# Optimization experiments

Measured on AMD Instinct MI355X. Metric: run time of the kernel, lower is better.

Reference implementation:

```python
import jax, jax.numpy as jnp
import numpy as np

NLIG = 16384
NPROT = 131072
N = NLIG + NPROT
E = 2097152
B = 256
H = 64


def setup_inputs() -> dict:
    key = jax.random.key(0)
    ks = jax.random.split(key, 40)
    i = iter(range(40))

    def nrm(shape, scale=0.1):
        return (jax.random.normal(ks[next(i)], shape, jnp.float32) * scale)

    inp = {
        'lig_pos': nrm((NLIG, 3), 1.0),
        'lig_feat': nrm((NLIG, 15), 1.0),
        'prot_pos': nrm((NPROT, 3), 1.0),
        'prot_feat': nrm((NPROT, 8), 1.0),
        't': jax.random.uniform(ks[next(i)], (B,), jnp.float32) * 1000.0,
        'lig_batch': jnp.sort(jax.random.randint(ks[next(i)], (NLIG,), 0, B)),
        'prot_batch': jnp.sort(jax.random.randint(ks[next(i)], (NPROT,), 0, B)),
        'edge_index': jax.random.randint(ks[next(i)], (2, E), 0, N),
        'W_lig': nrm((15, H)), 'b_lig': nrm((H,)),
        'W_prot': nrm((8, H)), 'b_prot': nrm((H,)),
        'Wt1': nrm((H, H)), 'bt1': nrm((H,)),
        'Wt2': nrm((H, H)), 'bt2': nrm((H,)),
        'Wrel1': nrm((H, H)), 'brel1': nrm((H,)), 'Wroot1': nrm((H, H)),
        'Wrel2': nrm((H, H)), 'brel2': nrm((H,)), 'Wroot2': nrm((H, H)),
        'Wrel3': nrm((H, H)), 'brel3': nrm((H,)), 'Wroot3': nrm((H, H)),
        'Wro1': nrm((H, H)), 'bro1': nrm((H,)),
        'Wro2': nrm((H, 1)), 'bro2': nrm((1,)),
    }
    return inp


def _time_embedding(t, dim):
    half = dim // 2
    freqs = jnp.exp(jnp.arange(half, dtype=jnp.float32) * (-np.log(10000.0) / (half - 1)))
    e = t[:, None] * freqs[None, :]  # [B, half]
    return jnp.concatenate([jnp.sin(e), jnp.cos(e)], axis=-1)  # [B, dim]


def _silu(x):
    return x * jax.nn.sigmoid(x)


def _graph_conv(x, src, dst, Wrel, brel, Wroot):
    # PyG GraphConv (aggr='add'): lin_rel(sum_j x_j) + lin_root(x)
    agg = jax.ops.segment_sum(x[src], dst, num_segments=N)  # [N, H]
    return agg @ Wrel + brel + x @ Wroot


def reference(lig_pos, lig_feat, prot_pos, prot_feat, t, lig_batch, prot_batch,
              edge_index, W_lig, b_lig, W_prot, b_prot, Wt1, bt1, Wt2, bt2,
              Wrel1, brel1, Wroot1, Wrel2, brel2, Wroot2, Wrel3, brel3, Wroot3,
              Wro1, bro1, Wro2, bro2):
    t_emb = _time_embedding(t, H)                      # [B, H]
    t_emb = _silu(t_emb @ Wt1 + bt1) @ Wt2 + bt2       # time_mlp
    x_lig = lig_feat @ W_lig + b_lig + t_emb[lig_batch]
    x_prot = prot_feat @ W_prot + b_prot
    x = jnp.concatenate([x_lig, x_prot], axis=0)       # [N, H]

    src, dst = edge_index[0], edge_index[1]
    x = _graph_conv(x, src, dst, Wrel1, brel1, Wroot1)
    x = _graph_conv(x, src, dst, Wrel2, brel2, Wroot2)
    x = _graph_conv(x, src, dst, Wrel3, brel3, Wroot3)

    # global_mean_pool over ligand nodes
    lig_x = x[:NLIG]
    sums = jax.ops.segment_sum(lig_x, lig_batch, num_segments=B)  # [B, H]
    cnt = jax.ops.segment_sum(jnp.ones((NLIG,), jnp.float32), lig_batch, num_segments=B)
    pooled = sums / jnp.maximum(cnt, 1.0)[:, None]

    return _silu(pooled @ Wro1 + bro1) @ Wro2 + bro2   # [B, 1]
```

## Files before the change

kernel.cpp:

```cpp
#include <hip/hip_runtime.h>
#include <math.h>

#define NLIG 16384
#define NPROT 131072
#define NTOT (NLIG + NPROT)
#define NEDGE 2097152
#define NB 256
#define H 64
#define NBUCK 576
#define BSHIFT 8
#define BCAP 4608
#define NPW 24

typedef short v4s __attribute__((ext_vector_type(4)));
typedef float v4f __attribute__((ext_vector_type(4)));

__device__ __forceinline__ unsigned short f2bf(float f) {
    unsigned int u = __float_as_uint(f);
    u += 0x7fff + ((u >> 16) & 1);
    return (unsigned short)(u >> 16);
}
__device__ __forceinline__ float bf2f(unsigned short s) {
    return __uint_as_float(((unsigned int)s) << 16);
}
__device__ __forceinline__ float bflo(unsigned int u) {
    return __uint_as_float(u << 16);
}
__device__ __forceinline__ float bfhi(unsigned int u) {
    return __uint_as_float(u & 0xffff0000u);
}

__global__ void time_mlp_kernel(const float* __restrict__ t,
                                const float* __restrict__ Wt1, const float* __restrict__ bt1,
                                const float* __restrict__ Wt2, const float* __restrict__ bt2,
                                float* __restrict__ t_emb) {
    int b = blockIdx.x;
    int h = threadIdx.x;
    __shared__ float emb_s[H];
    __shared__ float h1_s[H];
    float tv = t[b];
    int i = h & 31;
    float freq = expf((float)i * (-9.2103403719761836f / 31.0f));
    float e = tv * freq;
    emb_s[h] = (h < 32) ? sinf(e) : cosf(e);
    __syncthreads();
    float acc = bt1[h];
    #pragma unroll 8
    for (int k = 0; k < H; k++) acc += emb_s[k] * Wt1[k * H + h];
    float sig = 1.0f / (1.0f + expf(-acc));
    h1_s[h] = acc * sig;
    __syncthreads();
    float acc2 = bt2[h];
    #pragma unroll 8
    for (int k = 0; k < H; k++) acc2 += h1_s[k] * Wt2[k * H + h];
    t_emb[b * H + h] = acc2;
}

__global__ void wswz_kernel(const float* __restrict__ W0, const float* __restrict__ W1,
                            const float* __restrict__ W2, const float* __restrict__ W3,
                            const float* __restrict__ W4, const float* __restrict__ W5,
                            unsigned short* __restrict__ wbuf) {
    const float* Ws[6] = {W0, W1, W2, W3, W4, W5};
    int m = blockIdx.y;
    int t = blockIdx.x * 256 + threadIdx.x;
    int f = t >> 8, l = (t >> 2) & 63, i = t & 3;
    int kt = f >> 2, ct = f & 3;
    int row = 16 * kt + 4 * (l >> 4) + i;
    int col = 16 * ct + (l & 15);
    wbuf[m * 4096 + t] = f2bf(Ws[m][row * H + col]);
}

__global__ void node_init_kernel(const float* __restrict__ lig_feat,
                                 const float* __restrict__ prot_feat,
                                 const int* __restrict__ lig_batch,
                                 const float* __restrict__ t_emb,
                                 const float* __restrict__ W_lig, const float* __restrict__ b_lig,
                                 const float* __restrict__ W_prot, const float* __restrict__ b_prot,
                                 unsigned int* __restrict__ xb) {
    int node = blockIdx.x * 4 + (threadIdx.x >> 6);
    int h = threadIdx.x & 63;
    if (node >= NTOT) return;
    float acc;
    if (node < NLIG) {
        int b = lig_batch[node];
        acc = b_lig[h] + t_emb[b * H + h];
        #pragma unroll
        for (int k = 0; k < 15; k++)
            acc += lig_feat[node * 15 + k] * W_lig[k * H + h];
    } else {
        int p = node - NLIG;
        acc = b_prot[h];
        #pragma unroll
        for (int k = 0; k < 8; k++)
            acc += prot_feat[p * 8 + k] * W_prot[k * H + h];
    }
    float e0 = __shfl(acc, 2 * (h & 31));
    float e1 = __shfl(acc, 2 * (h & 31) + 1);
    if (h < 32)
        xb[node * 32 + h] = (unsigned int)f2bf(e0) | ((unsigned int)f2bf(e1) << 16);
}

__global__ __launch_bounds__(1024) void bucket_fill_kernel(const int* __restrict__ edge_index,
                                                           unsigned int* __restrict__ bcursor,
                                                           unsigned int* __restrict__ bucketed) {
    __shared__ unsigned int lh[NBUCK];
    __shared__ unsigned int lcur[NBUCK];
    __shared__ unsigned int gb[NBUCK];
    int tid = threadIdx.x;
    for (int i = tid; i < NBUCK; i += 1024) lh[i] = 0;
    __syncthreads();
    int e0 = blockIdx.x * 8192;
    int src[8], dst[8];
    #pragma unroll
    for (int k = 0; k < 8; k++) {
        src[k] = edge_index[e0 + k * 1024 + tid];
        dst[k] = edge_index[NEDGE + e0 + k * 1024 + tid];
        atomicAdd(&lh[dst[k] >> BSHIFT], 1);
    }
    __syncthreads();
    if (tid < NBUCK) {
        gb[tid] = atomicAdd(&bcursor[tid], lh[tid]);
        lcur[tid] = 0;
    }
    __syncthreads();
    #pragma unroll
    for (int k = 0; k < 8; k++) {
        int b = dst[k] >> BSHIFT;
        unsigned int r = atomicAdd(&lcur[b], 1);
        unsigned int slot = gb[b] + r;
        if (slot < BCAP)
            bucketed[b * BCAP + slot] = (unsigned int)src[k] | ((unsigned int)(dst[k] & 255) << 18);
    }
}

__global__ __launch_bounds__(512) void bucket_csr_kernel(const unsigned int* __restrict__ bucketed,
                                                         const unsigned int* __restrict__ bcursor,
                                                         int* __restrict__ off,
                                                         int* __restrict__ ends,
                                                         int* __restrict__ csr_src) {
    __shared__ unsigned int stage[BCAP];
    __shared__ unsigned int csr_l[BCAP];
    __shared__ unsigned int lh[256];
    __shared__ unsigned int lbeg[512];
    __shared__ unsigned int lcur[256];
    int b = blockIdx.x, tid = threadIdx.x;
    unsigned int base = (unsigned int)b * BCAP;
    int cnt = (int)bcursor[b];
    if (cnt > BCAP) cnt = BCAP;
    for (int i = tid; i < 256; i += 512) lh[i] = 0;
    __syncthreads();
    for (int i = tid; i < cnt; i += 512) {
        unsigned int v = bucketed[base + i];
        stage[i] = v;
        atomicAdd(&lh[v >> 18], 1);
    }
    __syncthreads();
    unsigned int own = (tid < 256) ? lh[tid] : 0;
    lbeg[tid] = own;
    __syncthreads();
    for (int d = 1; d < 512; d <<= 1) {
        unsigned int v = (tid >= d) ? lbeg[tid - d] : 0;
        __syncthreads();
        lbeg[tid] += v;
        __syncthreads();
    }
    unsigned int excl = lbeg[tid] - own;
    __syncthreads();
    lbeg[tid] = excl;
    if (tid < 256) {
        lcur[tid] = excl;
        off[b * 256 + tid]  = (int)(base + excl);
        ends[b * 256 + tid] = (int)(base + excl + own);
    }
    __syncthreads();
    for (int i = tid; i < cnt; i += 512) {
        unsigned int v = stage[i];
        unsigned int p = atomicAdd(&lcur[v >> 18], 1);
        csr_l[p] = v & 0x3ffffu;
    }
    __syncthreads();
    for (int i = tid; i < cnt; i += 512)
        csr_src[base + i] = (int)csr_l[i];
}

#define ACC8(u)                                   \
    do {                                          \
        a0 += bflo((u).x); a1 += bfhi((u).x);     \
        a2 += bflo((u).y); a3 += bfhi((u).y);     \
        a4 += bflo((u).z); a5 += bfhi((u).z);     \
        a6 += bflo((u).w); a7 += bfhi((u).w);     \
    } while (0)

#define DO_GROUP(BEG, DEG, IDFIRST, AGGROW)                                     \
    {                                                                           \
        int idcur = (IDFIRST);                                                  \
        float a0 = 0.f, a1 = 0.f, a2 = 0.f, a3 = 0.f;                           \
        float a4 = 0.f, a5 = 0.f, a6 = 0.f, a7 = 0.f;                           \
        for (int jb = 0; jb < (DEG); jb += 8) {                                 \
            int idnxt = (jb + 8 + q < (DEG)) ? csr[(BEG) + jb + 8 + q] : -1;    \
            int n0 = __shfl(idcur, s * 8 + 0);                                  \
            int n1 = __shfl(idcur, s * 8 + 1);                                  \
            int n2 = __shfl(idcur, s * 8 + 2);                                  \
            int n3 = __shfl(idcur, s * 8 + 3);                                  \
            int n4 = __shfl(idcur, s * 8 + 4);                                  \
            int n5 = __shfl(idcur, s * 8 + 5);                                  \
            int n6 = __shfl(idcur, s * 8 + 6);                                  \
            int n7 = __shfl(idcur, s * 8 + 7);                                  \
            int c1 = (n1 >= 0) ? n1 : n0;                                       \
            int c2 = (n2 >= 0) ? n2 : n0;                                       \
            int c3 = (n3 >= 0) ? n3 : n0;                                       \
            int c4 = (n4 >= 0) ? n4 : n0;                                       \
            int c5 = (n5 >= 0) ? n5 : n0;                                       \
            int c6 = (n6 >= 0) ? n6 : n0;                                       \
            int c7 = (n7 >= 0) ? n7 : n0;                                       \
            uint4 u0 = *(const uint4*)&xb[n0 * 32 + q * 4];                     \
            uint4 u1 = *(const uint4*)&xb[c1 * 32 + q * 4];                     \
            uint4 u2 = *(const uint4*)&xb[c2 * 32 + q * 4];                     \
            uint4 u3 = *(const uint4*)&xb[c3 * 32 + q * 4];                     \
            uint4 u4 = *(const uint4*)&xb[c4 * 32 + q * 4];                     \
            uint4 u5 = *(const uint4*)&xb[c5 * 32 + q * 4];                     \
            uint4 u6 = *(const uint4*)&xb[c6 * 32 + q * 4];                     \
            uint4 u7 = *(const uint4*)&xb[c7 * 32 + q * 4];                     \
            if (n1 < 0) { u1.x = u1.y = u1.z = u1.w = 0; }                      \
            if (n2 < 0) { u2.x = u2.y = u2.z = u2.w = 0; }                      \
            if (n3 < 0) { u3.x = u3.y = u3.z = u3.w = 0; }                      \
            if (n4 < 0) { u4.x = u4.y = u4.z = u4.w = 0; }                      \
            if (n5 < 0) { u5.x = u5.y = u5.z = u5.w = 0; }                      \
            if (n6 < 0) { u6.x = u6.y = u6.z = u6.w = 0; }                      \
            if (n7 < 0) { u7.x = u7.y = u7.z = u7.w = 0; }                      \
            ACC8(u0); ACC8(u1); ACC8(u2); ACC8(u3);                             \
            ACC8(u4); ACC8(u5); ACC8(u6); ACC8(u7);                             \
            idcur = idnxt;                                                      \
        }                                                                       \
        unsigned int p0 = (unsigned int)f2bf(a0) | ((unsigned int)f2bf(a1) << 16); \
        unsigned int p1 = (unsigned int)f2bf(a2) | ((unsigned int)f2bf(a3) << 16); \
        unsigned int p2 = (unsigned int)f2bf(a4) | ((unsigned int)f2bf(a5) << 16); \
        unsigned int p3 = (unsigned int)f2bf(a6) | ((unsigned int)f2bf(a7) << 16); \
        *(uint4*)&agg_s[(AGGROW) * 72 + q * 8] = make_uint4(p0, p1, p2, p3);    \
    }

__global__ __launch_bounds__(512, 6) void conv_kernel(const int* __restrict__ off,
                                                      const int* __restrict__ ends,
                                                      const int* __restrict__ csr,
                                                      const unsigned int* __restrict__ xb,
                                                      const unsigned short* __restrict__ wbuf,
                                                      const float* __restrict__ brel,
                                                      unsigned int* __restrict__ xob) {
    __shared__ unsigned int wlds[4096];
    __shared__ unsigned short agg_s[8 * NPW * 72];
    const int tid = threadIdx.x;
    const int w = tid >> 6, l = tid & 63;
    const unsigned int* wsrc = (const unsigned int*)wbuf;
    #pragma unroll
    for (int i = 0; i < 8; i++) wlds[i * 512 + tid] = wsrc[i * 512 + tid];

    const int s = l >> 3, q = l & 7;
    const int lrow = l & 15, g16 = l >> 4, g4 = 4 * (l >> 4);
    const int gwid = blockIdx.x * 8 + w;
    const int node0w = gwid * NPW;

    int bvv = (l < NPW) ? off[node0w + l] : 0;
    int evv = (l < NPW) ? ends[node0w + l] : 0;

    int b0 = __shfl(bvv, s),      d0 = __shfl(evv, s) - b0;
    int b1 = __shfl(bvv, 8 + s),  d1 = __shfl(evv, 8 + s) - b1;
    int b2 = __shfl(bvv, 16 + s), d2 = __shfl(evv, 16 + s) - b2;
    int id0 = (q < d0) ? csr[b0 + q] : -1;
    int id1 = (q < d1) ? csr[b1 + q] : -1;
    int id2 = (q < d2) ? csr[b2 + q] : -1;

    __syncthreads();

    float bv[4];
    #pragma unroll
    for (int ct = 0; ct < 4; ct++) bv[ct] = brel[ct * 16 + lrow];

    DO_GROUP(b0, d0, id0, w * NPW + s)
    DO_GROUP(b1, d1, id1, w * NPW + 8 + s)
    DO_GROUP(b2, d2, id2, w * NPW + 16 + s)

    __builtin_amdgcn_wave_barrier();

    v4s ax[4];
    #pragma unroll
    for (int kt = 0; kt < 4; kt++)
        ax[kt] = *(const v4s*)&xb[(node0w + lrow) * 32 + kt * 8 + g16 * 2];
    v4f acc[4];
    #pragma unroll
    for (int ct = 0; ct < 4; ct++) acc[ct] = (v4f){0.f, 0.f, 0.f, 0.f};
    #pragma unroll
    for (int kt = 0; kt < 4; kt++) {
        v4s a_agg = *(const v4s*)&agg_s[(w * NPW + lrow) * 72 + kt * 16 + g4];
        #pragma unroll
        for (int ct = 0; ct < 4; ct++) {
            int f = kt * 4 + ct;
            v4s wr = *(const v4s*)&wlds[f * 128 + l * 2];
            v4s wo = *(const v4s*)&wlds[2048 + f * 128 + l * 2];
            acc[ct] = __builtin_amdgcn_mfma_f32_16x16x16bf16_1k(a_agg, wr, acc[ct], 0, 0, 0);
            acc[ct] = __builtin_amdgcn_mfma_f32_16x16x16bf16_1k(ax[kt], wo, acc[ct], 0, 0, 0);
        }
    }
    const int r2row = 16 + (l & 7);
    v4s ax2[4];
    #pragma unroll
    for (int kt = 0; kt < 4; kt++)
        ax2[kt] = *(const v4s*)&xb[(node0w + r2row) * 32 + kt * 8 + g16 * 2];
    v4f acc2[4];
    #pragma unroll
    for (int ct = 0; ct < 4; ct++) acc2[ct] = (v4f){0.f, 0.f, 0.f, 0.f};
    #pragma unroll
    for (int kt = 0; kt < 4; kt++) {
        v4s a_agg2 = *(const v4s*)&agg_s[(w * NPW + r2row) * 72 + kt * 16 + g4];
        #pragma unroll
        for (int ct = 0; ct < 4; ct++) {
            int f = kt * 4 + ct;
            v4s wr = *(const v4s*)&wlds[f * 128 + l * 2];
            v4s wo = *(const v4s*)&wlds[2048 + f * 128 + l * 2];
            acc2[ct] = __builtin_amdgcn_mfma_f32_16x16x16bf16_1k(a_agg2, wr, acc2[ct], 0, 0, 0);
            acc2[ct] = __builtin_amdgcn_mfma_f32_16x16x16bf16_1k(ax2[kt], wo, acc2[ct], 0, 0, 0);
        }
    }
    __builtin_amdgcn_wave_barrier();

    #pragma unroll
    for (int ct = 0; ct < 4; ct++) {
        #pragma unroll
        for (int r = 0; r < 4; r++)
            agg_s[(w * NPW + g4 + r) * 72 + ct * 16 + lrow] = f2bf(acc[ct][r] + bv[ct]);
    }
    if (g16 < 2) {
        #pragma unroll
        for (int ct = 0; ct < 4; ct++) {
            #pragma unroll
            for (int r = 0; r < 4; r++)
                agg_s[(w * NPW + 16 + g4 + r) * 72 + ct * 16 + lrow] =
                    f2bf(acc2[ct][r] + bv[ct]);
        }
    }
    __builtin_amdgcn_wave_barrier();

    {
        int row = l >> 2, qq = l & 3;
        const unsigned int* srcp = (const unsigned int*)&agg_s[(w * NPW + row) * 72 + qq * 16];
        uint4 v0 = *(const uint4*)(srcp);
        uint4 v1 = *(const uint4*)(srcp + 4);
        *(uint4*)&xob[(node0w + row) * 32 + qq * 8] = v0;
        *(uint4*)&xob[(node0w + row) * 32 + qq * 8 + 4] = v1;
    }
    {
        int row = 16 + (l >> 3), qq = l & 7;
        *(uint4*)&xob[(node0w + row) * 32 + qq * 4] =
            *(const uint4*)&agg_s[(w * NPW + row) * 72 + qq * 8];
    }
}

__global__ __launch_bounds__(512, 6) void conv_lig_kernel(const int* __restrict__ off,
                                                          const int* __restrict__ ends,
                                                          const int* __restrict__ csr,
                                                          const unsigned int* __restrict__ xb,
                                                          const unsigned short* __restrict__ wbuf,
                                                          const float* __restrict__ brel,
                                                          const int* __restrict__ lig_batch,
                                                          float* __restrict__ pooled,
                                                          float* __restrict__ cnt) {
    __shared__ unsigned int wlds[4096];
    __shared__ unsigned short agg_s[8 * 8 * 72];
    const int tid = threadIdx.x;
    const int w = tid >> 6, l = tid & 63;
    const unsigned int* wsrc = (const unsigned int*)wbuf;
    #pragma unroll
    for (int i = 0; i < 8; i++) wlds[i * 512 + tid] = wsrc[i * 512 + tid];

    const int s = l >> 3, q = l & 7;
    const int lrow = l & 15, g16 = l >> 4, g4 = 4 * (l >> 4);
    const int gwid = blockIdx.x * 8 + w;
    const int node0w = gwid * 8;

    int bvv = (l < 8) ? off[node0w + l] : 0;
    int evv = (l < 8) ? ends[node0w + l] : 0;
    int b0 = __shfl(bvv, s), d0 = __shfl(evv, s) - b0;
    int id0 = (q < d0) ? csr[b0 + q] : -1;

    __syncthreads();

    float bv[4];
    #pragma unroll
    for (int ct = 0; ct < 4; ct++) bv[ct] = brel[ct * 16 + lrow];

    DO_GROUP(b0, d0, id0, w * 8 + s)

    __builtin_amdgcn_wave_barrier();

    const int arow = lrow & 7;
    v4s ax[4];
    #pragma unroll
    for (int kt = 0; kt < 4; kt++)
        ax[kt] = *(const v4s*)&xb[(node0w + arow) * 32 + kt * 8 + g16 * 2];
    v4f acc[4];
    #pragma unroll
    for (int ct = 0; ct < 4; ct++) acc[ct] = (v4f){0.f, 0.f, 0.f, 0.f};
    #pragma unroll
    for (int kt = 0; kt < 4; kt++) {
        v4s a_agg = *(const v4s*)&agg_s[(w * 8 + arow) * 72 + kt * 16 + g4];
        #pragma unroll
        for (int ct = 0; ct < 4; ct++) {
            int f = kt * 4 + ct;
            v4s wr = *(const v4s*)&wlds[f * 128 + l * 2];
            v4s wo = *(const v4s*)&wlds[2048 + f * 128 + l * 2];
            acc[ct] = __builtin_amdgcn_mfma_f32_16x16x16bf16_1k(a_agg, wr, acc[ct], 0, 0, 0);
            acc[ct] = __builtin_amdgcn_mfma_f32_16x16x16bf16_1k(ax[kt], wo, acc[ct], 0, 0, 0);
        }
    }

    if (g16 < 2) {
        #pragma unroll
        for (int r = 0; r < 4; r++) {
            int node = node0w + g4 + r;
            int bb = lig_batch[node];
            #pragma unroll
            for (int ct = 0; ct < 4; ct++)
                unsafeAtomicAdd(&pooled[bb * H + ct * 16 + lrow], acc[ct][r] + bv[ct]);
            if (lrow == 0) unsafeAtomicAdd(&cnt[bb], 1.0f);
        }
    }
}

__global__ void readout_kernel(const float* __restrict__ pooled, const float* __restrict__ cnt,
                               const float* __restrict__ Wro1, const float* __restrict__ bro1,
                               const float* __restrict__ Wro2, const float* __restrict__ bro2,
                               float* __restrict__ out) {
    __shared__ float pm[4][H];
    int w = threadIdx.x >> 6;
    int h = threadIdx.x & 63;
    int b = blockIdx.x * 4 + w;
    float c = fmaxf(cnt[b], 1.0f);
    pm[w][h] = pooled[b * H + h] / c;
    __syncthreads();
    float acc = bro1[h];
    #pragma unroll 8
    for (int k = 0; k < H; k++) acc += pm[w][k] * Wro1[k * H + h];
    float sig = 1.0f / (1.0f + expf(-acc));
    float s = acc * sig;
    float r = s * Wro2[h];
    #pragma unroll
    for (int off = 32; off; off >>= 1) r += __shfl_down(r, off);
    if (h == 0) out[b] = r + bro2[0];
}

extern "C" void kernel_launch(void* const* d_in, const int* in_sizes, int n_in,
                              void* d_out, int out_size, void* d_ws, size_t ws_size,
                              hipStream_t stream) {
    const float* lig_feat  = (const float*)d_in[1];
    const float* prot_feat = (const float*)d_in[3];
    const float* t         = (const float*)d_in[4];
    const int*   lig_batch = (const int*)d_in[5];
    const int*   edge_index= (const int*)d_in[7];
    const float* W_lig  = (const float*)d_in[8];
    const float* b_lig  = (const float*)d_in[9];
    const float* W_prot = (const float*)d_in[10];
    const float* b_prot = (const float*)d_in[11];
    const float* Wt1 = (const float*)d_in[12];
    const float* bt1 = (const float*)d_in[13];
    const float* Wt2 = (const float*)d_in[14];
    const float* bt2 = (const float*)d_in[15];
    const float* Wrel[3]  = {(const float*)d_in[16], (const float*)d_in[19], (const float*)d_in[22]};
    const float* brel[3]  = {(const float*)d_in[17], (const float*)d_in[20], (const float*)d_in[23]};
    const float* Wroot[3] = {(const float*)d_in[18], (const float*)d_in[21], (const float*)d_in[24]};
    const float* Wro1 = (const float*)d_in[25];
    const float* bro1 = (const float*)d_in[26];
    const float* Wro2 = (const float*)d_in[27];
    const float* bro2 = (const float*)d_in[28];
    float* out = (float*)d_out;

    char* ws = (char*)d_ws;
    int*            off_a   = (int*)(ws);
    int*            ends_a  = (int*)(ws + 655360);
    unsigned int*   bcursor = (unsigned int*)(ws + 1310720);
    float*          t_emb   = (float*)(ws + 1376256);
    float*          pooled  = (float*)(ws + 1441792);
    float*          cnt     = (float*)(ws + 1507328);
    unsigned short* wbuf    = (unsigned short*)(ws + 1572864);
    int*            csr_src = (int*)(ws + 2097152);
    unsigned int*   bucketed= (unsigned int*)(ws + 14680064);
    unsigned int*   xb0     = (unsigned int*)(ws + 27262976);
    unsigned int*   xb1     = (unsigned int*)(ws + 46137344);

    time_mlp_kernel<<<NB, H, 0, stream>>>(t, Wt1, bt1, Wt2, bt2, t_emb);
    wswz_kernel<<<dim3(16, 6), 256, 0, stream>>>(Wrel[0], Wroot[0], Wrel[1], Wroot[1],
                                                 Wrel[2], Wroot[2], wbuf);
    node_init_kernel<<<NTOT / 4, 256, 0, stream>>>(lig_feat, prot_feat, lig_batch, t_emb,
                                                   W_lig, b_lig, W_prot, b_prot, xb0);

    hipMemsetAsync(bcursor, 0, 2304, stream);
    bucket_fill_kernel<<<NEDGE / 8192, 1024, 0, stream>>>(edge_index, bcursor, bucketed);
    bucket_csr_kernel<<<NBUCK, 512, 0, stream>>>(bucketed, bcursor, off_a, ends_a, csr_src);

    hipMemsetAsync(pooled, 0, (size_t)(NB * H + NB) * sizeof(float), stream);

    conv_kernel<<<768, 512, 0, stream>>>(off_a, ends_a, csr_src, xb0,
                                         wbuf, brel[0], xb1);
    conv_kernel<<<768, 512, 0, stream>>>(off_a, ends_a, csr_src, xb1,
                                         wbuf + 8192, brel[1], xb0);
    conv_lig_kernel<<<NLIG / 64, 512, 0, stream>>>(off_a, ends_a, csr_src, xb0,
                                                   wbuf + 16384, brel[2], lig_batch,
                                                   pooled, cnt);

    readout_kernel<<<NB / 4, 256, 0, stream>>>(pooled, cnt, Wro1, bro1, Wro2, bro2, out);
}
```

Baseline: 219.9 us.

## Merge prep kernels and memsets into one launch, streamline bucket CSR build

Folds the time-MLP, weight swizzle and the two memsets (bucket cursors, pooled and count buffers) into a single prep kernel, cutting four launches down to one. The bucket CSR kernel now runs 1024 threads, scans only 256 entries, and scatters source indices directly to global memory instead of staging them in a second shared array. The direct scatter writes global memory at atomic-ordered positions, which is less coalesced than the previous staged copy.

```diff
diff --git a/kernel.cpp b/kernel.cpp
--- a/kernel.cpp
+++ b/kernel.cpp
@@ -30,44 +30,53 @@
     return __uint_as_float(u & 0xffff0000u);
 }
 
-__global__ void time_mlp_kernel(const float* __restrict__ t,
-                                const float* __restrict__ Wt1, const float* __restrict__ bt1,
-                                const float* __restrict__ Wt2, const float* __restrict__ bt2,
-                                float* __restrict__ t_emb) {
-    int b = blockIdx.x;
-    int h = threadIdx.x;
-    __shared__ float emb_s[H];
-    __shared__ float h1_s[H];
-    float tv = t[b];
-    int i = h & 31;
-    float freq = expf((float)i * (-9.2103403719761836f / 31.0f));
-    float e = tv * freq;
-    emb_s[h] = (h < 32) ? sinf(e) : cosf(e);
-    __syncthreads();
-    float acc = bt1[h];
-    #pragma unroll 8
-    for (int k = 0; k < H; k++) acc += emb_s[k] * Wt1[k * H + h];
-    float sig = 1.0f / (1.0f + expf(-acc));
-    h1_s[h] = acc * sig;
-    __syncthreads();
-    float acc2 = bt2[h];
-    #pragma unroll 8
-    for (int k = 0; k < H; k++) acc2 += h1_s[k] * Wt2[k * H + h];
-    t_emb[b * H + h] = acc2;
-}
-
-__global__ void wswz_kernel(const float* __restrict__ W0, const float* __restrict__ W1,
-                            const float* __restrict__ W2, const float* __restrict__ W3,
-                            const float* __restrict__ W4, const float* __restrict__ W5,
-                            unsigned short* __restrict__ wbuf) {
-    const float* Ws[6] = {W0, W1, W2, W3, W4, W5};
-    int m = blockIdx.y;
-    int t = blockIdx.x * 256 + threadIdx.x;
-    int f = t >> 8, l = (t >> 2) & 63, i = t & 3;
-    int kt = f >> 2, ct = f & 3;
-    int row = 16 * kt + 4 * (l >> 4) + i;
-    int col = 16 * ct + (l & 15);
-    wbuf[m * 4096 + t] = f2bf(Ws[m][row * H + col]);
+__global__ __launch_bounds__(256) void prep_kernel(const float* __restrict__ t,
+                                                   const float* __restrict__ Wt1, const float* __restrict__ bt1,
+                                                   const float* __restrict__ Wt2, const float* __restrict__ bt2,
+                                                   const float* __restrict__ W0, const float* __restrict__ W1,
+                                                   const float* __restrict__ W2, const float* __restrict__ W3,
+                                                   const float* __restrict__ W4, const float* __restrict__ W5,
+                                                   unsigned short* __restrict__ wbuf,
+                                                   float* __restrict__ t_emb,
+                                                   unsigned int* __restrict__ bcursor,
+                                                   float* __restrict__ pooled) {
+    int b = blockIdx.x, tid = threadIdx.x;
+    if (b < 96) {
+        const float* Ws[6] = {W0, W1, W2, W3, W4, W5};
+        int m = b >> 4;
+        int tt = (b & 15) * 256 + tid;
+        int f = tt >> 8, l = (tt >> 2) & 63, i = tt & 3;
+        int kt = f >> 2, ct = f & 3;
+        int row = 16 * kt + 4 * (l >> 4) + i;
+        int col = 16 * ct + (l & 15);
+        wbuf[m * 4096 + tt] = f2bf(Ws[m][row * H + col]);
+    } else if (b < 160) {
+        __shared__ float emb_s[4][H];
+        __shared__ float h1_s[4][H];
+        int w = tid >> 6, h = tid & 63;
+        int bb = (b - 96) * 4 + w;
+        float tv = t[bb];
+        int i = h & 31;
+        float freq = expf((float)i * (-9.2103403719761836f / 31.0f));
+        float e = tv * freq;
+        emb_s[w][h] = (h < 32) ? sinf(e) : cosf(e);
+        __syncthreads();
+        float acc = bt1[h];
+        #pragma unroll 8
+        for (int k = 0; k < H; k++) acc += emb_s[w][k] * Wt1[k * H + h];
+        float sig = 1.0f / (1.0f + expf(-acc));
+        h1_s[w][h] = acc * sig;
+        __syncthreads();
+        float acc2 = bt2[h];
+        #pragma unroll 8
+        for (int k = 0; k < H; k++) acc2 += h1_s[w][k] * Wt2[k * H + h];
+        t_emb[bb * H + h] = acc2;
+    } else {
+        int idx = (b - 160) * 256 + tid;
+        if (idx < NBUCK) bcursor[idx] = 0;
+        int idx2 = idx - NBUCK;
+        if (idx2 >= 0 && idx2 < NB * H + NB) pooled[idx2] = 0.0f;
+    }
 }
 
 __global__ void node_init_kernel(const float* __restrict__ lig_feat,
@@ -133,54 +142,48 @@
     }
 }
 
-__global__ __launch_bounds__(512) void bucket_csr_kernel(const unsigned int* __restrict__ bucketed,
-                                                         const unsigned int* __restrict__ bcursor,
-                                                         int* __restrict__ off,
-                                                         int* __restrict__ ends,
-                                                         int* __restrict__ csr_src) {
+__global__ __launch_bounds__(1024) void bucket_csr_kernel(const unsigned int* __restrict__ bucketed,
+                                                          const unsigned int* __restrict__ bcursor,
+                                                          int* __restrict__ off,
+                                                          int* __restrict__ ends,
+                                                          int* __restrict__ csr_src) {
     __shared__ unsigned int stage[BCAP];
-    __shared__ unsigned int csr_l[BCAP];
     __shared__ unsigned int lh[256];
-    __shared__ unsigned int lbeg[512];
+    __shared__ unsigned int sc[256];
     __shared__ unsigned int lcur[256];
     int b = blockIdx.x, tid = threadIdx.x;
     unsigned int base = (unsigned int)b * BCAP;
     int cnt = (int)bcursor[b];
     if (cnt > BCAP) cnt = BCAP;
-    for (int i = tid; i < 256; i += 512) lh[i] = 0;
-    __syncthreads();
-    for (int i = tid; i < cnt; i += 512) {
+    if (tid < 256) lh[tid] = 0;
+    __syncthreads();
+    for (int i = tid; i < cnt; i += 1024) {
         unsigned int v = bucketed[base + i];
         stage[i] = v;
         atomicAdd(&lh[v >> 18], 1);
     }
     __syncthreads();
-    unsigned int own = (tid < 256) ? lh[tid] : 0;
-    lbeg[tid] = own;
-    __syncthreads();
-    for (int d = 1; d < 512; d <<= 1) {
-        unsigned int v = (tid >= d) ? lbeg[tid - d] : 0;
+    if (tid < 256) sc[tid] = lh[tid];
+    __syncthreads();
+    #pragma unroll
+    for (int d = 1; d < 256; d <<= 1) {
+        unsigned int v = (tid < 256 && tid >= (unsigned)d) ? sc[tid - d] : 0;
         __syncthreads();
-        lbeg[tid] += v;
+        if (tid < 256) sc[tid] += v;
         __syncthreads();
     }
-    unsigned int excl = lbeg[tid] - own;
-    __syncthreads();
-    lbeg[tid] = excl;
     if (tid < 256) {
+        unsigned int excl = sc[tid] - lh[tid];
         lcur[tid] = excl;
         off[b * 256 + tid]  = (int)(base + excl);
-        ends[b * 256 + tid] = (int)(base + excl + own);
-    }
-    __syncthreads();
-    for (int i = tid; i < cnt; i += 512) {
+        ends[b * 256 + tid] = (int)(base + excl + lh[tid]);
+    }
+    __syncthreads();
+    for (int i = tid; i < cnt; i += 1024) {
         unsigned int v = stage[i];
         unsigned int p = atomicAdd(&lcur[v >> 18], 1);
-        csr_l[p] = v & 0x3ffffu;
-    }
-    __syncthreads();
-    for (int i = tid; i < cnt; i += 512)
-        csr_src[base + i] = (int)csr_l[i];
+        csr_src[base + p] = (int)(v & 0x3ffffu);
+    }
 }
 
 #define ACC8(u)                                   \
@@ -485,17 +488,15 @@
     unsigned int*   xb0     = (unsigned int*)(ws + 27262976);
     unsigned int*   xb1     = (unsigned int*)(ws + 46137344);
 
-    time_mlp_kernel<<<NB, H, 0, stream>>>(t, Wt1, bt1, Wt2, bt2, t_emb);
-    wswz_kernel<<<dim3(16, 6), 256, 0, stream>>>(Wrel[0], Wroot[0], Wrel[1], Wroot[1],
-                                                 Wrel[2], Wroot[2], wbuf);
+    prep_kernel<<<228, 256, 0, stream>>>(t, Wt1, bt1, Wt2, bt2,
+                                         Wrel[0], Wroot[0], Wrel[1], Wroot[1], Wrel[2], Wroot[2],
+                                         wbuf, t_emb, bcursor, pooled);
+
     node_init_kernel<<<NTOT / 4, 256, 0, stream>>>(lig_feat, prot_feat, lig_batch, t_emb,
                                                    W_lig, b_lig, W_prot, b_prot, xb0);
 
-    hipMemsetAsync(bcursor, 0, 2304, stream);
     bucket_fill_kernel<<<NEDGE / 8192, 1024, 0, stream>>>(edge_index, bcursor, bucketed);
-    bucket_csr_kernel<<<NBUCK, 512, 0, stream>>>(bucketed, bcursor, off_a, ends_a, csr_src);
-
-    hipMemsetAsync(pooled, 0, (size_t)(NB * H + NB) * sizeof(float), stream);
+    bucket_csr_kernel<<<NBUCK, 1024, 0, stream>>>(bucketed, bcursor, off_a, ends_a, csr_src);
 
     conv_kernel<<<768, 512, 0, stream>>>(off_a, ends_a, csr_src, xb0,
                                          wbuf, brel[0], xb1);
```

After: 222.1 us. Within noise of the previous version (+1.0%).
